# Optimization experiments

Measured on AMD Instinct MI355X. Metric: run time of the kernel, lower is better.

The kernel has to match this reference:

```python
import jax, jax.numpy as jnp
import numpy as np

D_MODEL = 1024
NUM_HEADS = 16
D_K = D_MODEL // NUM_HEADS
R = 8
ALPHA = 16
SCALING = ALPHA / R


def _lora_linear(x, W, b, A, Bm):
    # base: x @ W.T + b ; lora: (x @ A.T) @ Bm.T * scaling
    base = jnp.einsum('btd,od->bto', x, W) + b
    lora = jnp.einsum('btr,or->bto', jnp.einsum('btd,rd->btr', x, A), Bm) * SCALING
    return base + lora


def setup_inputs() -> dict:
    key = jax.random.key(0)
    ks = jax.random.split(key, 20)
    B, T = 2, 2048
    inp = {
        'q': jax.random.normal(ks[0], (B, T, D_MODEL), jnp.float32),
        'k': jax.random.normal(ks[1], (B, T, D_MODEL), jnp.float32),
        'v': jax.random.normal(ks[2], (B, T, D_MODEL), jnp.float32),
        'mask': jnp.ones((1, 1, T, T), jnp.int32),
    }
    i = 3
    for name in ('q', 'k', 'v'):
        inp[f'W{name}'] = jax.random.normal(ks[i], (D_MODEL, D_MODEL), jnp.float32) * 0.02; i += 1
        inp[f'b{name}'] = jnp.zeros((D_MODEL,), jnp.float32)
        inp[f'A{name}'] = jax.random.normal(ks[i], (R, D_MODEL), jnp.float32) * 0.01; i += 1
        inp[f'B{name}'] = jax.random.normal(ks[i], (D_MODEL, R), jnp.float32) * 0.01; i += 1
    inp['Wo'] = jax.random.normal(ks[i], (D_MODEL, D_MODEL), jnp.float32) * 0.02
    inp['bo'] = jnp.zeros((D_MODEL,), jnp.float32)
    return inp


def reference(q, k, v, mask, Wq, bq, Aq, Bq, Wk, bk, Ak, Bk, Wv, bv, Av, Bv, Wo, bo):
    B, Tq, _ = q.shape
    Tk = k.shape[1]
    Q = _lora_linear(q, Wq, bq, Aq, Bq).reshape(B, Tq, NUM_HEADS, D_K).transpose(0, 2, 1, 3)
    K = _lora_linear(k, Wk, bk, Ak, Bk).reshape(B, Tk, NUM_HEADS, D_K).transpose(0, 2, 1, 3)
    V = _lora_linear(v, Wv, bv, Av, Bv).reshape(B, Tk, NUM_HEADS, D_K).transpose(0, 2, 1, 3)
    scores = jnp.einsum('bhqd,bhkd->bhqk', Q, K) / jnp.sqrt(jnp.float32(D_K))
    scores = jnp.where(mask == 0, jnp.float32(-1e9), scores)
    attn = jax.nn.softmax(scores, axis=-1)
    out = jnp.einsum('bhqk,bhkd->bhqd', attn, V)
    out = out.transpose(0, 2, 1, 3).reshape(B, Tq, D_MODEL)
    return jnp.einsum('btd,od->bto', out, Wo) + bo
```

## Files before the change

### kernel.cpp

```cpp
#include <hip/hip_runtime.h>
#include <stdint.h>

typedef unsigned short u16;
typedef __attribute__((ext_vector_type(4))) float f32x4;
typedef __attribute__((ext_vector_type(4))) uint32_t u32x4;
typedef __attribute__((ext_vector_type(8))) __bf16 bf16x8;

#if __has_builtin(__builtin_amdgcn_exp2f)
#define EXP2(x) __builtin_amdgcn_exp2f(x)
#else
#define EXP2(x) exp2f(x)
#endif

static __device__ __forceinline__ u16 f2bf(float f) {
    union { float f; uint32_t i; } v; v.f = f;
    return (u16)((v.i + 0x7FFFu + ((v.i >> 16) & 1u)) >> 16);
}
static __device__ __forceinline__ uint32_t cvtpk(float lo, float hi) {
    uint32_t r;
    asm("v_cvt_pk_bf16_f32 %0, %1, %2" : "=v"(r) : "v"(lo), "v"(hi));
    return r;
}

static __device__ __forceinline__ void gl2lds16(const u16* g, u16* lds) {
    __builtin_amdgcn_global_load_lds(
        (const __attribute__((address_space(1))) void*)g,
        (__attribute__((address_space(3))) void*)lds, 16, 0, 0);
}

struct PrepArgs {
    const float* x[3]; const float* A[3]; float* o[3]; u16* xb[3];
    const float* wsrc[4]; u16* wdst[4];
    const int* mask; int* flags;
};

__global__ __launch_bounds__(256)
void prep_kernel(PrepArgs a) {
    const int bid = blockIdx.x;
    const int tid = threadIdx.x;

    if (bid < 3072) {
        const int z = bid >> 10;
        const int row = (bid & 1023) * 4 + (tid >> 6);
        const int lane = tid & 63;
        const float* xr = a.x[z] + (size_t)row * 1024 + lane * 16;
        float xv[16];
#pragma unroll
        for (int j = 0; j < 4; ++j) *(float4*)&xv[j * 4] = *(const float4*)(xr + j * 4);
        {
            u16 ob[16];
#pragma unroll
            for (int j = 0; j < 16; ++j) ob[j] = f2bf(xv[j]);
            u16* dp = a.xb[z] + (size_t)row * 1024 + lane * 16;
            *(uint4*)dp = *(const uint4*)&ob[0];
            *(uint4*)(dp + 8) = *(const uint4*)&ob[8];
        }
        float s[8];
#pragma unroll
        for (int r = 0; r < 8; ++r) {
            const float* ar = a.A[z] + (size_t)r * 1024 + lane * 16;
            float av[16];
#pragma unroll
            for (int j = 0; j < 4; ++j) *(float4*)&av[j * 4] = *(const float4*)(ar + j * 4);
            float acc = 0.f;
#pragma unroll
            for (int j = 0; j < 16; ++j) acc += xv[j] * av[j];
#pragma unroll
            for (int off = 1; off < 64; off <<= 1) acc += __shfl_xor(acc, off, 64);
            s[r] = acc;
        }
        if (lane == 0) {
#pragma unroll
            for (int r = 0; r < 8; ++r) a.o[z][(size_t)row * 8 + r] = s[r];
        }
    } else if (bid < 3328) {
        const int b2 = bid - 3072;
        const int arr = b2 >> 6, boff = b2 & 63;
        const float* s = a.wsrc[arr] + (size_t)boff * 16384;
        u16* d = a.wdst[arr] + (size_t)boff * 16384;
#pragma unroll
        for (int i = 0; i < 8; ++i) {
            int c = tid + i * 256;
            float4 f0 = *(const float4*)(s + c * 8);
            float4 f1 = *(const float4*)(s + c * 8 + 4);
            u16 o[8];
            o[0] = f2bf(f0.x); o[1] = f2bf(f0.y); o[2] = f2bf(f0.z); o[3] = f2bf(f0.w);
            o[4] = f2bf(f1.x); o[5] = f2bf(f1.y); o[6] = f2bf(f1.z); o[7] = f2bf(f1.w);
            *(uint4*)(d + c * 8) = *(const uint4*)o;
        }
    } else {
        const int b3 = bid - 3328;
        const int qb = b3 & 15, kt = b3 >> 4;
        int ok = 1;
#pragma unroll
        for (int i = 0; i < 8; ++i) {
            int c = tid + i * 256;
            int row = c >> 4, cg = c & 15;
            int4 m4 = *(const int4*)&a.mask[(size_t)(qb * 128 + row) * 2048 + kt * 64 + cg * 4];
            ok &= (m4.x != 0) & (m4.y != 0) & (m4.z != 0) & (m4.w != 0);
        }
        int wall = __all(ok) ? 1 : 0;
        __shared__ int red[4];
        if ((tid & 63) == 0) red[tid >> 6] = wall;
        __syncthreads();
        if (tid == 0) a.flags[qb * 32 + kt] = red[0] & red[1] & red[2] & red[3];
    }
}

struct GemmPtrs { const u16* X; const u16* W; const float* bias; const float* XA; const float* Bm; void* out; int transT; float oscale; };
struct GemmArgs { GemmPtrs p[3]; };

#define LST 136
#define LTT 72

template <int WMT, int WNT, int LORA>
__global__ __launch_bounds__(256, 2)
void gemm_kernel(GemmArgs args) {
    constexpr int BM = WMT * 32, BN = WNT * 32;
    constexpr int MBLK = 4096 / BM;
    constexpr int IPA = BM / 32;
    constexpr int IPB = BN / 32;
    __shared__ alignas(16) u16 smem[(BM + BN) * 64];
    u16* As = smem;
    u16* Bs = smem + BM * 64;

    const GemmPtrs gp = args.p[blockIdx.z];
    const int tid = threadIdx.x;
    const int lane = tid & 63, wave = tid >> 6;
    const int wm = wave >> 1, wn = wave & 1;
    const int l15 = lane & 15, l4 = lane >> 4;
    const int id = blockIdx.x;
    const int m0 = (id % MBLK) * BM, n0 = (id / MBLK) * BN;

    const int srow = lane >> 3;
    const int scol = ((lane & 7) ^ srow) * 8;
    const u16* gA[IPA];
    const u16* gB[IPB];
#pragma unroll
    for (int i = 0; i < IPA; ++i) {
        int q = wave * IPA + i;
        gA[i] = gp.X + (size_t)(m0 + q * 8 + srow) * 1024 + scol;
    }
#pragma unroll
    for (int i = 0; i < IPB; ++i) {
        int q = wave * IPB + i;
        gB[i] = gp.W + (size_t)(n0 + q * 8 + srow) * 1024 + scol;
    }

    const f32x4 fz = {0.f, 0.f, 0.f, 0.f};
    f32x4 acc[WMT][WNT];
#pragma unroll
    for (int i = 0; i < WMT; ++i)
#pragma unroll
        for (int j = 0; j < WNT; ++j) acc[i][j] = fz;

    const int sw = l15 & 7;
    for (int kb = 0; kb < 16; ++kb) {
        __syncthreads();
#pragma unroll
        for (int i = 0; i < IPA; ++i)
            gl2lds16(gA[i] + kb * 64, &As[(wave * IPA + i) * 512]);
#pragma unroll
        for (int i = 0; i < IPB; ++i)
            gl2lds16(gB[i] + kb * 64, &Bs[(wave * IPB + i) * 512]);
        __syncthreads();
#pragma unroll
        for (int kk2 = 0; kk2 < 2; ++kk2) {
            bf16x8 af[WMT], bfr[WNT];
#pragma unroll
            for (int mt = 0; mt < WMT; ++mt) {
                int x = wm * (WMT * 16) + mt * 16 + l15;
                af[mt] = *(const bf16x8*)&As[x * 64 + (((kk2 * 4 + l4) ^ sw) * 8)];
            }
#pragma unroll
            for (int nt = 0; nt < WNT; ++nt) {
                int y = wn * (WNT * 16) + nt * 16 + l15;
                bfr[nt] = *(const bf16x8*)&Bs[y * 64 + (((kk2 * 4 + l4) ^ sw) * 8)];
            }
#pragma unroll
            for (int mt = 0; mt < WMT; ++mt)
#pragma unroll
                for (int nt = 0; nt < WNT; ++nt)
                    acc[mt][nt] = __builtin_amdgcn_mfma_f32_16x16x32_bf16(af[mt], bfr[nt], acc[mt][nt], 0, 0, 0);
        }
    }

    if constexpr (LORA) {
        __syncthreads();
        float* XAs = (float*)smem;
        float* Bms = (float*)(smem + BM * 64);
        {
            int rr = tid >> 1, hf = (tid & 1) * 4;
            *(float4*)&XAs[rr * 8 + hf] = *(const float4*)&gp.XA[(size_t)(m0 + rr) * 8 + hf];
            if (tid < 128) {
                *(float4*)&Bms[tid * 8]     = *(const float4*)&gp.Bm[(size_t)(n0 + tid) * 8];
                *(float4*)&Bms[tid * 8 + 4] = *(const float4*)&gp.Bm[(size_t)(n0 + tid) * 8 + 4];
            }
        }
        __syncthreads();
        const float osc = gp.oscale;
        float bmv[WNT][8], bsv[WNT];
#pragma unroll
        for (int nt = 0; nt < WNT; ++nt) {
            int nloc = wn * 64 + nt * 16 + l15;
            bsv[nt] = gp.bias[n0 + nloc];
#pragma unroll
            for (int q8 = 0; q8 < 8; ++q8) bmv[nt][q8] = Bms[nloc * 8 + q8];
        }
#pragma unroll
        for (int mt = 0; mt < WMT; ++mt)
#pragma unroll
            for (int r = 0; r < 4; ++r) {
                int mloc = wm * 64 + mt * 16 + l4 * 4 + r;
                float xa8[8];
                *(float4*)&xa8[0] = *(const float4*)&XAs[mloc * 8];
                *(float4*)&xa8[4] = *(const float4*)&XAs[mloc * 8 + 4];
#pragma unroll
                for (int nt = 0; nt < WNT; ++nt) {
                    float lora = 0.f;
#pragma unroll
                    for (int q8 = 0; q8 < 8; ++q8) lora += xa8[q8] * bmv[nt][q8];
                    acc[mt][nt][r] = (acc[mt][nt][r] + bsv[nt] + 2.0f * lora) * osc;
                }
            }
        __syncthreads();

        u16* outp = (u16*)gp.out;
        const int bb = m0 >> 11;
        if (gp.transT) {
            u16* Lst = smem;
#pragma unroll
            for (int ch = 0; ch < 2; ++ch) {
#pragma unroll
                for (int mt2 = 0; mt2 < 2; ++mt2) {
                    int mt = ch * 2 + mt2;
#pragma unroll
                    for (int nt = 0; nt < WNT; ++nt)
#pragma unroll
                        for (int r = 0; r < 4; ++r)
                            Lst[(wn * 64 + nt * 16 + l15) * LTT + wm * 32 + mt2 * 16 + l4 * 4 + r] =
                                f2bf(acc[mt][nt][r]);
                }
                __syncthreads();
#pragma unroll
                for (int j = 0; j < 4; ++j) {
                    int w = tid + j * 256;
                    int nl = w >> 3, seg = w & 7;
                    uint4 val = *(const uint4*)&Lst[nl * LTT + seg * 8];
                    int n = n0 + nl, hh = n >> 6, dd = n & 63;
                    int c0 = seg * 8;
                    int gm = m0 + (c0 >> 5) * 64 + ch * 32 + (c0 & 31);
                    int t = gm & 2047;
                    *(uint4*)&outp[(((size_t)(bb * 16 + hh)) * 64 + dd) * 2048 + t] = val;
                }
                __syncthreads();
            }
        } else {
            u16* Ls = smem;
#pragma unroll
            for (int ch = 0; ch < 2; ++ch) {
#pragma unroll
                for (int mt2 = 0; mt2 < 2; ++mt2) {
                    int mt = ch * 2 + mt2;
#pragma unroll
                    for (int nt = 0; nt < WNT; ++nt)
#pragma unroll
                        for (int r = 0; r < 4; ++r)
                            Ls[(wm * 32 + mt2 * 16 + l4 * 4 + r) * LST + wn * 64 + nt * 16 + l15] =
                                f2bf(acc[mt][nt][r]);
                }
                __syncthreads();
#pragma unroll
                for (int j = 0; j < 4; ++j) {
                    int w = tid + j * 256;
                    int lrow = w >> 4, seg = w & 15;
                    uint4 val = *(const uint4*)&Ls[lrow * LST + seg * 8];
                    int gm = m0 + (lrow >> 5) * 64 + ch * 32 + (lrow & 31);
                    int t = gm & 2047;
                    int n = n0 + seg * 8, hh = n >> 6, dd = n & 63;
                    *(uint4*)&outp[(((size_t)(bb * 16 + hh)) * 2048 + t) * 64 + dd] = val;
                }
                __syncthreads();
            }
        }
    } else {
        float* outp = (float*)gp.out;
#pragma unroll
        for (int mt = 0; mt < WMT; ++mt)
#pragma unroll
            for (int r = 0; r < 4; ++r) {
                int m = m0 + wm * (WMT * 16) + mt * 16 + l4 * 4 + r;
#pragma unroll
                for (int nt = 0; nt < WNT; ++nt) {
                    int n = n0 + wn * (WNT * 16) + nt * 16 + l15;
                    outp[(size_t)m * 1024 + n] = acc[mt][nt][r] + gp.bias[n];
                }
            }
    }
}


__global__ __launch_bounds__(256, 4)
void attn_kernel(const u16* __restrict__ QKV, const int* __restrict__ mask,
                 const int* __restrict__ flags, u16* __restrict__ Xo) {
    const int qb = blockIdx.x >> 5;
    const int bh = blockIdx.x & 31;
    const int b = bh >> 4, h = bh & 15;
    const int tid = threadIdx.x;
    const int lane = tid & 63, wave = tid >> 6;
    const int l15 = lane & 15, l4 = lane >> 4;

    __shared__ alignas(16) u16 Ks[2][64 * 64];
    __shared__ alignas(16) u16 Vts[2][64 * 64];

    const size_t plane = (size_t)2 * 16 * 2048 * 64;
    const u16* Qg = QKV + (size_t)(b * 16 + h) * 2048 * 64;
    const u16* Kg = Qg + plane;
    const u16* Vg = Kg + plane;

    const int srow = lane >> 3;
    const int scol = ((lane & 7) ^ srow) * 8;

    const u16* kbase[2];
    const u16* vbase[2];
#pragma unroll
    for (int i = 0; i < 2; ++i) {
        int qq = wave * 2 + i;
        int kc = 16 * (qq & 1) + 8 * (srow >> 2) + 4 * ((qq >> 1) & 1) + (srow & 3) + 32 * (qq >> 2);
        kbase[i] = Kg + (size_t)kc * 64 + scol;
        vbase[i] = Vg + (size_t)(qq * 8 + srow) * 2048 + scol;
    }

    bf16x8 qa[2];
#pragma unroll
    for (int kk2 = 0; kk2 < 2; ++kk2)
        qa[kk2] = *(const bf16x8*)&Qg[(size_t)(qb * 64 + wave * 16 + l15) * 64 + kk2 * 32 + l4 * 8];

    const f32x4 fz = {0.f, 0.f, 0.f, 0.f};
    f32x4 accO[4];
#pragma unroll
    for (int dt = 0; dt < 4; ++dt) accO[dt] = fz;
    float lsum = 0.f;

#pragma unroll
    for (int i = 0; i < 2; ++i) {
        int qq = wave * 2 + i;
        gl2lds16(kbase[i], &Ks[0][qq * 512]);
        gl2lds16(vbase[i], &Vts[0][qq * 512]);
    }
    __syncthreads();

    for (int kt = 0; kt < 32; ++kt) {
        const u16* Kc = &Ks[kt & 1][0];
        const u16* Vc = &Vts[kt & 1][0];

        if (kt < 31) {
            u16* Kn = &Ks[(kt + 1) & 1][0];
            u16* Vn = &Vts[(kt + 1) & 1][0];
#pragma unroll
            for (int i = 0; i < 2; ++i) {
                int qq = wave * 2 + i;
                gl2lds16(kbase[i] + (size_t)(kt + 1) * 4096, &Kn[qq * 512]);
                gl2lds16(vbase[i] + (size_t)(kt + 1) * 64, &Vn[qq * 512]);
            }
        }

        f32x4 accS[4];
#pragma unroll
        for (int j = 0; j < 4; ++j) accS[j] = fz;
#pragma unroll
        for (int kk2 = 0; kk2 < 2; ++kk2) {
            bf16x8 kf[4];
#pragma unroll
            for (int j = 0; j < 4; ++j)
                kf[j] = *(const bf16x8*)&Kc[(j * 16 + l15) * 64 + (((kk2 * 4 + l4) ^ (l15 & 7)) * 8)];
            __builtin_amdgcn_s_setprio(1);
#pragma unroll
            for (int j = 0; j < 4; ++j)
                accS[j] = __builtin_amdgcn_mfma_f32_16x16x32_bf16(kf[j], qa[kk2], accS[j], 0, 0, 0);
            __builtin_amdgcn_s_setprio(0);
        }

        if (flags[(qb >> 1) * 32 + kt] == 0) {
            int qrow = qb * 64 + wave * 16 + l15;
#pragma unroll
            for (int j = 0; j < 4; ++j)
#pragma unroll
                for (int r = 0; r < 4; ++r) {
                    int kcol = kt * 64 + 8 * l4 + 4 * (j & 1) + r + 32 * (j >> 1);
                    if (mask[(size_t)qrow * 2048 + kcol] == 0) accS[j][r] = -1e9f;
                }
        }

        float part0 = 0.f, part1 = 0.f;
#pragma unroll
        for (int j = 0; j < 4; ++j)
#pragma unroll
            for (int r = 0; r < 4; ++r) {
                float p = EXP2(accS[j][r]);
                accS[j][r] = p;
                if (j & 1) part1 += p; else part0 += p;
            }
        lsum += part0 + part1;

        u32x4 paw0, paw1;
        paw0[0] = cvtpk(accS[0][0], accS[0][1]); paw0[1] = cvtpk(accS[0][2], accS[0][3]);
        paw0[2] = cvtpk(accS[1][0], accS[1][1]); paw0[3] = cvtpk(accS[1][2], accS[1][3]);
        paw1[0] = cvtpk(accS[2][0], accS[2][1]); paw1[1] = cvtpk(accS[2][2], accS[2][3]);
        paw1[2] = cvtpk(accS[3][0], accS[3][1]); paw1[3] = cvtpk(accS[3][2], accS[3][3]);
        bf16x8 pa[2];
        pa[0] = __builtin_bit_cast(bf16x8, paw0);
        pa[1] = __builtin_bit_cast(bf16x8, paw1);

#pragma unroll
        for (int kk2 = 0; kk2 < 2; ++kk2) {
            bf16x8 vf[4];
#pragma unroll
            for (int dt = 0; dt < 4; ++dt)
                vf[dt] = *(const bf16x8*)&Vc[(dt * 16 + l15) * 64 + (((kk2 * 4 + l4) ^ (l15 & 7)) * 8)];
            __builtin_amdgcn_s_setprio(1);
#pragma unroll
            for (int dt = 0; dt < 4; ++dt)
                accO[dt] = __builtin_amdgcn_mfma_f32_16x16x32_bf16(pa[kk2], vf[dt], accO[dt], 0, 0, 0);
            __builtin_amdgcn_s_setprio(0);
        }

        __syncthreads();
    }

    float tot = lsum;
    tot += __shfl_xor(tot, 16, 64);
    tot += __shfl_xor(tot, 32, 64);
    float inv[4];
#pragma unroll
    for (int r = 0; r < 4; ++r) inv[r] = 1.0f / __shfl(tot, l4 * 4 + r, 64);

    u16* Es = &Ks[0][0];
#pragma unroll
    for (int dt = 0; dt < 4; ++dt)
#pragma unroll
        for (int r = 0; r < 4; ++r) {
            int prow = wave * 16 + l4 * 4 + r;
            Es[prow * 64 + (((dt * 2 + (l15 >> 3)) ^ (prow & 7)) * 8) + (l15 & 7)] =
                f2bf(accO[dt][r] * inv[r]);
        }
    __syncthreads();
#pragma unroll
    for (int j = 0; j < 2; ++j) {
        int w = tid + j * 256;
        int row = w >> 3, seg = w & 7;
        uint4 val = *(const uint4*)&Es[row * 64 + ((seg ^ (row & 7)) * 8)];
        int t = qb * 64 + row;
        *(uint4*)&Xo[((size_t)(b * 2048 + t)) * 1024 + h * 64 + seg * 8] = val;
    }
}

extern "C" void kernel_launch(void* const* d_in, const int* in_sizes, int n_in,
                              void* d_out, int out_size, void* d_ws, size_t ws_size,
                              hipStream_t stream) {
    const float* q    = (const float*)d_in[0];
    const float* k    = (const float*)d_in[1];
    const float* v    = (const float*)d_in[2];
    const int*   mask = (const int*)d_in[3];
    const float* Wq = (const float*)d_in[4];
    const float* bq = (const float*)d_in[5];
    const float* Aq = (const float*)d_in[6];
    const float* Bq = (const float*)d_in[7];
    const float* Wk = (const float*)d_in[8];
    const float* bk = (const float*)d_in[9];
    const float* Ak = (const float*)d_in[10];
    const float* Bk = (const float*)d_in[11];
    const float* Wv = (const float*)d_in[12];
    const float* bv = (const float*)d_in[13];
    const float* Av = (const float*)d_in[14];
    const float* Bv = (const float*)d_in[15];
    const float* Wo = (const float*)d_in[16];
    const float* bo = (const float*)d_in[17];

    char* ws = (char*)d_ws;
    u16*   QKV   = (u16*)ws;
    u16*   qb16  = (u16*)(ws + 25165824);
    u16*   kb16  = (u16*)(ws + 33554432);
    u16*   vb16  = (u16*)(ws + 41943040);
    u16*   Wqb   = (u16*)(ws + 50331648);
    u16*   Wkb   = (u16*)(ws + 52428800);
    u16*   Wvb   = (u16*)(ws + 54525952);
    u16*   Wob   = (u16*)(ws + 56623104);
    float* XAbuf = (float*)(ws + 58720256);
    int*   flags = (int*)(ws + 59113472);
    u16*   Xbuf  = qb16;

    PrepArgs pa;
    pa.x[0] = q;  pa.x[1] = k;  pa.x[2] = v;
    pa.A[0] = Aq; pa.A[1] = Ak; pa.A[2] = Av;
    pa.o[0] = XAbuf; pa.o[1] = XAbuf + 32768; pa.o[2] = XAbuf + 65536;
    pa.xb[0] = qb16; pa.xb[1] = kb16; pa.xb[2] = vb16;
    pa.wsrc[0] = Wq; pa.wsrc[1] = Wk; pa.wsrc[2] = Wv; pa.wsrc[3] = Wo;
    pa.wdst[0] = Wqb; pa.wdst[1] = Wkb; pa.wdst[2] = Wvb; pa.wdst[3] = Wob;
    pa.mask = mask; pa.flags = flags;
    prep_kernel<<<dim3(3840), dim3(256), 0, stream>>>(pa);

    const float QSCALE = 0.1803368801f;
    GemmArgs g1;
    g1.p[0] = GemmPtrs{qb16, Wqb, bq, XAbuf,         Bq, (void*)QKV,             0, QSCALE};
    g1.p[1] = GemmPtrs{kb16, Wkb, bk, XAbuf + 32768, Bk, (void*)(QKV + 4194304), 0, 1.0f};
    g1.p[2] = GemmPtrs{vb16, Wvb, bv, XAbuf + 65536, Bv, (void*)(QKV + 8388608), 1, 1.0f};
    gemm_kernel<4, 4, 1><<<dim3(256, 1, 3), dim3(256), 0, stream>>>(g1);

    attn_kernel<<<dim3(1024), dim3(256), 0, stream>>>(QKV, mask, flags, Xbuf);

    GemmArgs g2;
    g2.p[0] = GemmPtrs{Xbuf, Wob, bo, nullptr, nullptr, d_out, 0, 1.0f};
    g2.p[1] = g2.p[0];
    g2.p[2] = g2.p[0];
    gemm_kernel<2, 4, 0><<<dim3(512, 1, 1), dim3(256), 0, stream>>>(g2);
}
```

Baseline: 274.2 us.

## Fuse LoRA down-projection into QKV GEMM via extra MFMA on packed A

```diff
diff --git a/kernel.cpp b/kernel.cpp
--- a/kernel.cpp
+++ b/kernel.cpp
@@ -29,8 +29,8 @@
 }
 
 struct PrepArgs {
-    const float* x[3]; const float* A[3]; float* o[3]; u16* xb[3];
-    const float* wsrc[4]; u16* wdst[4];
+    const float* csrc[7]; u16* cdst[7];
+    const float* A[3]; u16* apk[3];
     const int* mask; int* flags;
 };
 
@@ -39,45 +39,12 @@
     const int bid = blockIdx.x;
     const int tid = threadIdx.x;
 
-    if (bid < 3072) {
-        const int z = bid >> 10;
-        const int row = (bid & 1023) * 4 + (tid >> 6);
-        const int lane = tid & 63;
-        const float* xr = a.x[z] + (size_t)row * 1024 + lane * 16;
-        float xv[16];
-#pragma unroll
-        for (int j = 0; j < 4; ++j) *(float4*)&xv[j * 4] = *(const float4*)(xr + j * 4);
-        {
-            u16 ob[16];
-#pragma unroll
-            for (int j = 0; j < 16; ++j) ob[j] = f2bf(xv[j]);
-            u16* dp = a.xb[z] + (size_t)row * 1024 + lane * 16;
-            *(uint4*)dp = *(const uint4*)&ob[0];
-            *(uint4*)(dp + 8) = *(const uint4*)&ob[8];
-        }
-        float s[8];
-#pragma unroll
-        for (int r = 0; r < 8; ++r) {
-            const float* ar = a.A[z] + (size_t)r * 1024 + lane * 16;
-            float av[16];
-#pragma unroll
-            for (int j = 0; j < 4; ++j) *(float4*)&av[j * 4] = *(const float4*)(ar + j * 4);
-            float acc = 0.f;
-#pragma unroll
-            for (int j = 0; j < 16; ++j) acc += xv[j] * av[j];
-#pragma unroll
-            for (int off = 1; off < 64; off <<= 1) acc += __shfl_xor(acc, off, 64);
-            s[r] = acc;
-        }
-        if (lane == 0) {
-#pragma unroll
-            for (int r = 0; r < 8; ++r) a.o[z][(size_t)row * 8 + r] = s[r];
-        }
-    } else if (bid < 3328) {
-        const int b2 = bid - 3072;
-        const int arr = b2 >> 6, boff = b2 & 63;
-        const float* s = a.wsrc[arr] + (size_t)boff * 16384;
-        u16* d = a.wdst[arr] + (size_t)boff * 16384;
+    if (bid < 1024) {
+        int arr, boff;
+        if (bid < 768) { arr = bid >> 8; boff = bid & 255; }
+        else { int b2 = bid - 768; arr = 3 + (b2 >> 6); boff = b2 & 63; }
+        const float* s = a.csrc[arr] + (size_t)boff * 16384;
+        u16* d = a.cdst[arr] + (size_t)boff * 16384;
 #pragma unroll
         for (int i = 0; i < 8; ++i) {
             int c = tid + i * 256;
@@ -88,8 +55,8 @@
             o[4] = f2bf(f1.x); o[5] = f2bf(f1.y); o[6] = f2bf(f1.z); o[7] = f2bf(f1.w);
             *(uint4*)(d + c * 8) = *(const uint4*)o;
         }
-    } else {
-        const int b3 = bid - 3328;
+    } else if (bid < 1536) {
+        const int b3 = bid - 1024;
         const int qb = b3 & 15, kt = b3 >> 4;
         int ok = 1;
 #pragma unroll
@@ -104,10 +71,30 @@
         if ((tid & 63) == 0) red[tid >> 6] = wall;
         __syncthreads();
         if (tid == 0) a.flags[qb * 32 + kt] = red[0] & red[1] & red[2] & red[3];
-    }
-}
-
-struct GemmPtrs { const u16* X; const u16* W; const float* bias; const float* XA; const float* Bm; void* out; int transT; float oscale; };
+    } else {
+        const int z = bid - 1536;
+        const float* Az = a.A[z];
+        u16* dp = a.apk[z];
+#pragma unroll
+        for (int i = 0; i < 8; ++i) {
+            int pos = tid + i * 256;
+            int lane2 = pos & 63;
+            int l15_ = lane2 & 15, l4_ = lane2 >> 4;
+            int kbkk = pos >> 6;
+            int kcol = (kbkk >> 1) * 64 + (kbkk & 1) * 32 + l4_ * 8;
+            u16 ob[8] = {0, 0, 0, 0, 0, 0, 0, 0};
+            if (l15_ < 8) {
+                float4 f0 = *(const float4*)&Az[(size_t)l15_ * 1024 + kcol];
+                float4 f1 = *(const float4*)&Az[(size_t)l15_ * 1024 + kcol + 4];
+                ob[0] = f2bf(f0.x); ob[1] = f2bf(f0.y); ob[2] = f2bf(f0.z); ob[3] = f2bf(f0.w);
+                ob[4] = f2bf(f1.x); ob[5] = f2bf(f1.y); ob[6] = f2bf(f1.z); ob[7] = f2bf(f1.w);
+            }
+            *(uint4*)&dp[(size_t)pos * 8] = *(const uint4*)ob;
+        }
+    }
+}
+
+struct GemmPtrs { const u16* X; const u16* W; const float* bias; const u16* Ap; const float* Bm; void* out; int transT; float oscale; };
 struct GemmArgs { GemmPtrs p[3]; };
 
 #define LST 136
@@ -153,6 +140,11 @@
     for (int i = 0; i < WMT; ++i)
 #pragma unroll
         for (int j = 0; j < WNT; ++j) acc[i][j] = fz;
+    f32x4 acc_xa[WMT];
+    if constexpr (LORA) {
+#pragma unroll
+        for (int i = 0; i < WMT; ++i) acc_xa[i] = fz;
+    }
 
     const int sw = l15 & 7;
     for (int kb = 0; kb < 16; ++kb) {
@@ -182,6 +174,12 @@
 #pragma unroll
                 for (int nt = 0; nt < WNT; ++nt)
                     acc[mt][nt] = __builtin_amdgcn_mfma_f32_16x16x32_bf16(af[mt], bfr[nt], acc[mt][nt], 0, 0, 0);
+            if constexpr (LORA) {
+                bf16x8 abf = *(const bf16x8*)&gp.Ap[(size_t)((kb * 2 + kk2) * 64 + lane) * 8];
+#pragma unroll
+                for (int mt = 0; mt < WMT; ++mt)
+                    acc_xa[mt] = __builtin_amdgcn_mfma_f32_16x16x32_bf16(af[mt], abf, acc_xa[mt], 0, 0, 0);
+            }
         }
     }
 
@@ -189,13 +187,16 @@
         __syncthreads();
         float* XAs = (float*)smem;
         float* Bms = (float*)(smem + BM * 64);
-        {
-            int rr = tid >> 1, hf = (tid & 1) * 4;
-            *(float4*)&XAs[rr * 8 + hf] = *(const float4*)&gp.XA[(size_t)(m0 + rr) * 8 + hf];
-            if (tid < 128) {
-                *(float4*)&Bms[tid * 8]     = *(const float4*)&gp.Bm[(size_t)(n0 + tid) * 8];
-                *(float4*)&Bms[tid * 8 + 4] = *(const float4*)&gp.Bm[(size_t)(n0 + tid) * 8 + 4];
-            }
+        if (wn == 0 && l15 < 8) {
+#pragma unroll
+            for (int mt = 0; mt < WMT; ++mt)
+#pragma unroll
+                for (int r = 0; r < 4; ++r)
+                    XAs[(wm * 64 + mt * 16 + l4 * 4 + r) * 8 + l15] = acc_xa[mt][r];
+        }
+        if (tid < 128) {
+            *(float4*)&Bms[tid * 8]     = *(const float4*)&gp.Bm[(size_t)(n0 + tid) * 8];
+            *(float4*)&Bms[tid * 8 + 4] = *(const float4*)&gp.Bm[(size_t)(n0 + tid) * 8 + 4];
         }
         __syncthreads();
         const float osc = gp.oscale;
@@ -486,25 +487,25 @@
     u16*   Wkb   = (u16*)(ws + 52428800);
     u16*   Wvb   = (u16*)(ws + 54525952);
     u16*   Wob   = (u16*)(ws + 56623104);
-    float* XAbuf = (float*)(ws + 58720256);
+    u16*   Apk   = (u16*)(ws + 58720256);
     int*   flags = (int*)(ws + 59113472);
     u16*   Xbuf  = qb16;
 
     PrepArgs pa;
-    pa.x[0] = q;  pa.x[1] = k;  pa.x[2] = v;
+    pa.csrc[0] = q;  pa.csrc[1] = k;  pa.csrc[2] = v;
+    pa.csrc[3] = Wq; pa.csrc[4] = Wk; pa.csrc[5] = Wv; pa.csrc[6] = Wo;
+    pa.cdst[0] = qb16; pa.cdst[1] = kb16; pa.cdst[2] = vb16;
+    pa.cdst[3] = Wqb;  pa.cdst[4] = Wkb;  pa.cdst[5] = Wvb; pa.cdst[6] = Wob;
     pa.A[0] = Aq; pa.A[1] = Ak; pa.A[2] = Av;
-    pa.o[0] = XAbuf; pa.o[1] = XAbuf + 32768; pa.o[2] = XAbuf + 65536;
-    pa.xb[0] = qb16; pa.xb[1] = kb16; pa.xb[2] = vb16;
-    pa.wsrc[0] = Wq; pa.wsrc[1] = Wk; pa.wsrc[2] = Wv; pa.wsrc[3] = Wo;
-    pa.wdst[0] = Wqb; pa.wdst[1] = Wkb; pa.wdst[2] = Wvb; pa.wdst[3] = Wob;
+    pa.apk[0] = Apk; pa.apk[1] = Apk + 16384; pa.apk[2] = Apk + 32768;
     pa.mask = mask; pa.flags = flags;
-    prep_kernel<<<dim3(3840), dim3(256), 0, stream>>>(pa);
+    prep_kernel<<<dim3(1539), dim3(256), 0, stream>>>(pa);
 
     const float QSCALE = 0.1803368801f;
     GemmArgs g1;
-    g1.p[0] = GemmPtrs{qb16, Wqb, bq, XAbuf,         Bq, (void*)QKV,             0, QSCALE};
-    g1.p[1] = GemmPtrs{kb16, Wkb, bk, XAbuf + 32768, Bk, (void*)(QKV + 4194304), 0, 1.0f};
-    g1.p[2] = GemmPtrs{vb16, Wvb, bv, XAbuf + 65536, Bv, (void*)(QKV + 8388608), 1, 1.0f};
+    g1.p[0] = GemmPtrs{qb16, Wqb, bq, Apk,         Bq, (void*)QKV,             0, QSCALE};
+    g1.p[1] = GemmPtrs{kb16, Wkb, bk, Apk + 16384, Bk, (void*)(QKV + 4194304), 0, 1.0f};
+    g1.p[2] = GemmPtrs{vb16, Wvb, bv, Apk + 32768, Bv, (void*)(QKV + 8388608), 1, 1.0f};
     gemm_kernel<4, 4, 1><<<dim3(256, 1, 3), dim3(256), 0, stream>>>(g1);
 
     attn_kernel<<<dim3(1024), dim3(256), 0, stream>>>(QKV, mask, flags, Xbuf);
```

After: 255.4 us. -6.9%, faster.
